# Kernel optimization log

Measured on AMD Instinct MI355X. Metric: run time of the kernel, lower is better.

## Reference

```python
import jax, jax.numpy as jnp
import numpy as np

NUM_EMBEDDINGS = 8192
EMBEDDING_DIM = 256
COMMITMENT_COST = 0.25
TAU = 0.9
B, C, H, W = 4, NUM_EMBEDDINGS, 32, 32


def setup_inputs() -> dict:
    key = jax.random.key(0)
    k1, k2, k3 = jax.random.split(key, 3)
    x = jax.random.normal(k1, (B, C, H, W), dtype=jnp.float32)
    # nn.Embedding weight initialized uniform(-0.5, 0.5)
    emb_weight = jax.random.uniform(k2, (NUM_EMBEDDINGS, EMBEDDING_DIM),
                                    dtype=jnp.float32, minval=-0.5, maxval=0.5)
    # standard Gumbel(0,1) noise, sampled once for reproducibility
    u = jax.random.uniform(k3, (B, C, H, W), dtype=jnp.float32,
                           minval=1e-10, maxval=1.0)
    gumbel_noise = -jnp.log(-jnp.log(u))
    return {"x": x, "emb_weight": emb_weight, "gumbel_noise": gumbel_noise}


def reference(x, emb_weight, gumbel_noise):
    n = x.shape[1]  # num_embeddings (channel dim)
    # --- gumbel_softmax(tau=0.9, hard=True, dim=1) ---
    y_soft = jax.nn.softmax((x + gumbel_noise) / TAU, axis=1)  # [B,N,H,W]
    idx = jnp.argmax(y_soft, axis=1)                           # [B,H,W]
    y_hard = jax.nn.one_hot(idx, n, axis=1, dtype=y_soft.dtype)
    # straight-through estimator
    one_hot = y_soft + jax.lax.stop_gradient(y_hard - y_soft)  # [B,N,H,W]
    # --- codebook lookup as one-hot matmul ---
    quantized = jnp.einsum('bnhw,nd->bdhw', one_hot, emb_weight)
    # --- KL(uniform || q) with F.kl_div semantics, reduction='batchmean' ---
    # logits rearranged to b (h w) n and log_softmax over n == log_softmax over axis=1 of x
    log_qy = jax.nn.log_softmax(x, axis=1)                     # [B,N,H,W]
    t = 1.0 / n
    # pointwise kl = target * (log(target) - log_qy); batchmean divides by B
    kl_div = jnp.sum(t * (jnp.log(jnp.asarray(t, x.dtype)) - log_qy)) / x.shape[0]
    return quantized, COMMITMENT_COST * kl_div, one_hot
```

## Files before the change

### kernel.cpp

```cpp
#include <hip/hip_runtime.h>
#include <math.h>

#define BSZ 4
#define CCH 8192
#define HW  1024
#define DEMB 256
#define NPOS (BSZ*HW)
#define QSIZE (BSZ*DEMB*HW)
#define KLOFF QSIZE
#define OHOFF (QSIZE+1)
#define OHSZ  ((size_t)BSZ*CCH*HW)

typedef float vf4 __attribute__((ext_vector_type(4)));

template<int CPB>
__global__ __launch_bounds__(256) void vq_phase1(const float* __restrict__ x,
                                                 const float* __restrict__ g,
                                                 float* __restrict__ out,
                                                 float* __restrict__ ws) {
    constexpr int NCH = CCH / CPB;
    constexpr int P   = NPOS * NCH;
    constexpr int UN  = 16;
    int bid = blockIdx.x;
    int q = bid % NCH;
    int b = bid / NCH;
    int t = threadIdx.x;
    int c0 = q * CPB;
    size_t base = ((size_t)(b * CCH + c0)) * HW + 4 * t;

    float best[4]; int bidx[4]; float s[4], sx[4];
#pragma unroll
    for (int j = 0; j < 4; j++) { best[j] = -INFINITY; bidx[j] = 0; s[j] = 0.f; sx[j] = 0.f; }

    const vf4 z4 = (vf4)(0.f);
    for (int cg = 0; cg < CPB / UN; cg++) {
        size_t a0 = base + (size_t)cg * UN * HW;
        vf4 xv[UN], gv[UN];
#pragma unroll
        for (int u = 0; u < UN; u++)
            xv[u] = __builtin_nontemporal_load((const vf4*)(x + a0 + (size_t)u * HW));
#pragma unroll
        for (int u = 0; u < UN; u++)
            gv[u] = __builtin_nontemporal_load((const vf4*)(g + a0 + (size_t)u * HW));
#pragma unroll
        for (int u = 0; u < UN; u++)
            __builtin_nontemporal_store(z4, (vf4*)(out + QSIZE + a0 + (size_t)u * HW));
#pragma unroll
        for (int u = 0; u < UN; u++) {
            int cc = c0 + cg * UN + u;
#pragma unroll
            for (int j = 0; j < 4; j++) {
                float xa = xv[u][j];
                float z = xa + gv[u][j];
                if (z > best[j]) { best[j] = z; bidx[j] = cc; }
                s[j]  += __expf(xa);
                sx[j] += xa;
            }
        }
    }

    if (b == BSZ - 1 && q == NCH - 1 && t == 255)
        out[QSIZE + OHSZ] = 0.f;

    int o = q * NPOS + b * HW + 4 * t;
    float* wbest = ws;
    int*   widx  = (int*)(ws + (size_t)P);
    float* wsum  = ws + 2 * (size_t)P;
    float* wsx   = ws + 3 * (size_t)P;
    *(float4*)(wbest + o) = make_float4(best[0], best[1], best[2], best[3]);
    *(int4*)  (widx  + o) = make_int4(bidx[0], bidx[1], bidx[2], bidx[3]);
    *(float4*)(wsum  + o) = make_float4(s[0], s[1], s[2], s[3]);
    *(float4*)(wsx   + o) = make_float4(sx[0], sx[1], sx[2], sx[3]);
}

template<int CPB>
__global__ __launch_bounds__(256) void vq_phase2(const float* __restrict__ emb,
                                                 float* __restrict__ out,
                                                 float* __restrict__ ws) {
    constexpr int NCH = CCH / CPB;
    constexpr int P   = NPOS * NCH;
    constexpr int QPT = NCH / 16;
    constexpr int TP  = 272;
    const float* wbest = ws;
    const int*   widx  = (const int*)(ws + (size_t)P);
    const float* wsum  = ws + 2 * (size_t)P;
    const float* wsx   = ws + 3 * (size_t)P;

    int tid = threadIdx.x;
    int pl = tid & 15;
    int qg = tid >> 4;
    int pos0 = blockIdx.x * 16;
    int pos = pos0 + pl;

    float fb = -INFINITY; int fi = 0;
    float fs = 0.f, fsx = 0.f;
    for (int i = 0; i < QPT; i++) {
        int q = qg * QPT + i;
        int o = q * NPOS + pos;
        float v = wbest[o]; int ci = widx[o];
        if (v > fb || (v == fb && ci < fi)) { fb = v; fi = ci; }
        fs  += wsum[o];
        fsx += wsx[o];
    }

    __shared__ float l_b [16][17];
    __shared__ int   l_i [16][17];
    __shared__ float l_s [16][17];
    __shared__ float l_sx[16][17];
    __shared__ float tsum[16];
    __shared__ int   smi[16];
    __shared__ float tile[16 * TP];
    l_b [qg][pl] = fb;
    l_i [qg][pl] = fi;
    l_s [qg][pl] = fs;
    l_sx[qg][pl] = fsx;
    __syncthreads();

    if (tid < 16) {
        int p = tid;
        float mb = l_b[0][p]; int mi = l_i[0][p];
        float ms = l_s[0][p], msx = l_sx[0][p];
        for (int qq = 1; qq < 16; qq++) {
            float v = l_b[qq][p]; int ci = l_i[qq][p];
            if (v > mb || (v == mb && ci < mi)) { mb = v; mi = ci; }
            ms  += l_s[qq][p];
            msx += l_sx[qq][p];
        }
        int mypos = pos0 + p;
        smi[p] = mi;
        int bb = mypos >> 10;
        int hw = mypos & (HW - 1);
        out[OHOFF + ((size_t)(bb * CCH + mi)) * HW + hw] = 1.0f;

        const float logt = -9.0109131783f;
        tsum[p] = logt + __logf(ms) - msx * (1.0f / (float)CCH);
    }
    __syncthreads();
    if (tid == 0) {
        float tt = 0.f;
        for (int p = 0; p < 16; p++) tt += tsum[p];
        atomicAdd(out + KLOFF, (0.25f / (float)BSZ) * tt);
    }

    int rr = tid >> 6;
    int c4 = (tid & 63) * 4;
#pragma unroll
    for (int rep = 0; rep < 4; rep++) {
        int r = rep * 4 + rr;
        float4 v = *(const float4*)(emb + (size_t)smi[r] * DEMB + c4);
        *(float4*)(tile + r * TP + c4) = v;
    }
    __syncthreads();

    int b = pos0 >> 10;
    int hw0 = pos0 & (HW - 1);
    int d = tid;
    size_t obase = (((size_t)(b * DEMB + d)) << 10) + hw0;
#pragma unroll
    for (int k = 0; k < 4; k++) {
        float4 v;
        v.x = tile[(4 * k + 0) * TP + d];
        v.y = tile[(4 * k + 1) * TP + d];
        v.z = tile[(4 * k + 2) * TP + d];
        v.w = tile[(4 * k + 3) * TP + d];
        *(float4*)(out + obase + 4 * k) = v;
    }
}

template<int CPB>
static void launch_all(const float* x, const float* emb, const float* g,
                       float* out, float* ws, hipStream_t stream) {
    constexpr int NCH = CCH / CPB;
    vq_phase1<CPB><<<dim3(BSZ * NCH), dim3(256), 0, stream>>>(x, g, out, ws);
    vq_phase2<CPB><<<dim3(NPOS / 16), dim3(256), 0, stream>>>(emb, out, ws);
}

extern "C" void kernel_launch(void* const* d_in, const int* in_sizes, int n_in,
                              void* d_out, int out_size, void* d_ws, size_t ws_size,
                              hipStream_t stream) {
    (void)in_sizes; (void)n_in; (void)out_size;
    const float* x   = (const float*)d_in[0];
    const float* emb = (const float*)d_in[1];
    const float* g   = (const float*)d_in[2];
    float* out = (float*)d_out;
    float* ws  = (float*)d_ws;

    if (ws_size >= (size_t)16 * ((size_t)NPOS * (CCH / 32))) {
        launch_all<32>(x, emb, g, out, ws, stream);
    } else {
        launch_all<64>(x, emb, g, out, ws, stream);
    }
}
```

Before: 325.1 us.

## Split phase1 blocks over spatial halves with float2 loads and cooperative zero stores

Measured after the change: 352.2 us. 8.3% more time.

```diff
diff --git a/kernel.cpp b/kernel.cpp
--- a/kernel.cpp
+++ b/kernel.cpp
@@ -12,6 +12,7 @@
 #define OHSZ  ((size_t)BSZ*CCH*HW)
 
 typedef float vf4 __attribute__((ext_vector_type(4)));
+typedef float vf2 __attribute__((ext_vector_type(2)));
 
 template<int CPB>
 __global__ __launch_bounds__(256) void vq_phase1(const float* __restrict__ x,
@@ -21,35 +22,46 @@
     constexpr int NCH = CCH / CPB;
     constexpr int P   = NPOS * NCH;
     constexpr int UN  = 16;
+    constexpr int HHW = HW / 2;
     int bid = blockIdx.x;
-    int q = bid % NCH;
-    int b = bid / NCH;
+    int h  = bid & 1;
+    int qb = bid >> 1;
+    int q = qb % NCH;
+    int b = qb / NCH;
     int t = threadIdx.x;
     int c0 = q * CPB;
-    size_t base = ((size_t)(b * CCH + c0)) * HW + 4 * t;
-
-    float best[4]; int bidx[4]; float s[4], sx[4];
-#pragma unroll
-    for (int j = 0; j < 4; j++) { best[j] = -INFINITY; bidx[j] = 0; s[j] = 0.f; sx[j] = 0.f; }
+    int hw0 = h * HHW;
+    size_t base = ((size_t)(b * CCH + c0)) * HW + hw0 + 2 * t;
+
+    float best[2]; int bidx[2]; float s[2], sx[2];
+#pragma unroll
+    for (int j = 0; j < 2; j++) { best[j] = -INFINITY; bidx[j] = 0; s[j] = 0.f; sx[j] = 0.f; }
 
     const vf4 z4 = (vf4)(0.f);
     for (int cg = 0; cg < CPB / UN; cg++) {
         size_t a0 = base + (size_t)cg * UN * HW;
-        vf4 xv[UN], gv[UN];
+        vf2 xv[UN], gv[UN];
 #pragma unroll
         for (int u = 0; u < UN; u++)
-            xv[u] = __builtin_nontemporal_load((const vf4*)(x + a0 + (size_t)u * HW));
+            xv[u] = *(const vf2*)(x + a0 + (size_t)u * HW);
 #pragma unroll
         for (int u = 0; u < UN; u++)
-            gv[u] = __builtin_nontemporal_load((const vf4*)(g + a0 + (size_t)u * HW));
-#pragma unroll
-        for (int u = 0; u < UN; u++)
-            __builtin_nontemporal_store(z4, (vf4*)(out + QSIZE + a0 + (size_t)u * HW));
+            gv[u] = *(const vf2*)(g + a0 + (size_t)u * HW);
+
+        size_t zb = ((size_t)(b * CCH + c0 + cg * UN)) * HW + hw0;
+#pragma unroll
+        for (int k = 0; k < 8; k++) {
+            int flat = k * 256 + t;
+            int cl   = flat >> 7;
+            int off4 = (flat & 127) * 4;
+            __builtin_nontemporal_store(z4, (vf4*)(out + QSIZE + zb + (size_t)cl * HW + off4));
+        }
+
 #pragma unroll
         for (int u = 0; u < UN; u++) {
             int cc = c0 + cg * UN + u;
 #pragma unroll
-            for (int j = 0; j < 4; j++) {
+            for (int j = 0; j < 2; j++) {
                 float xa = xv[u][j];
                 float z = xa + gv[u][j];
                 if (z > best[j]) { best[j] = z; bidx[j] = cc; }
@@ -59,18 +71,18 @@
         }
     }
 
-    if (b == BSZ - 1 && q == NCH - 1 && t == 255)
+    if (b == BSZ - 1 && q == NCH - 1 && h == 1 && t == 255)
         out[QSIZE + OHSZ] = 0.f;
 
-    int o = q * NPOS + b * HW + 4 * t;
+    int o = q * NPOS + b * HW + hw0 + 2 * t;
     float* wbest = ws;
     int*   widx  = (int*)(ws + (size_t)P);
     float* wsum  = ws + 2 * (size_t)P;
     float* wsx   = ws + 3 * (size_t)P;
-    *(float4*)(wbest + o) = make_float4(best[0], best[1], best[2], best[3]);
-    *(int4*)  (widx  + o) = make_int4(bidx[0], bidx[1], bidx[2], bidx[3]);
-    *(float4*)(wsum  + o) = make_float4(s[0], s[1], s[2], s[3]);
-    *(float4*)(wsx   + o) = make_float4(sx[0], sx[1], sx[2], sx[3]);
+    *(float2*)(wbest + o) = make_float2(best[0], best[1]);
+    *(int2*)  (widx  + o) = make_int2(bidx[0], bidx[1]);
+    *(float2*)(wsum  + o) = make_float2(s[0], s[1]);
+    *(float2*)(wsx   + o) = make_float2(sx[0], sx[1]);
 }
 
 template<int CPB>
@@ -171,7 +183,7 @@
 static void launch_all(const float* x, const float* emb, const float* g,
                        float* out, float* ws, hipStream_t stream) {
     constexpr int NCH = CCH / CPB;
-    vq_phase1<CPB><<<dim3(BSZ * NCH), dim3(256), 0, stream>>>(x, g, out, ws);
+    vq_phase1<CPB><<<dim3(BSZ * NCH * 2), dim3(256), 0, stream>>>(x, g, out, ws);
     vq_phase2<CPB><<<dim3(NPOS / 16), dim3(256), 0, stream>>>(emb, out, ws);
 }
 
```

## Replace per-chunk partial workspace with global atomic max/add reduction

Applied to the files above, without the earlier changes.

Result: slower. 383.5 us (+18.0%).

```diff
diff --git a/kernel.cpp b/kernel.cpp
--- a/kernel.cpp
+++ b/kernel.cpp
@@ -12,6 +12,13 @@
 #define OHSZ  ((size_t)BSZ*CCH*HW)
 
 typedef float vf4 __attribute__((ext_vector_type(4)));
+typedef unsigned long long u64;
+
+
+__global__ __launch_bounds__(256) void vq_init(float* __restrict__ ws) {
+    int i = blockIdx.x * 256 + threadIdx.x;
+    ((vf4*)ws)[i] = (vf4)(0.f);
+}
 
 template<int CPB>
 __global__ __launch_bounds__(256) void vq_phase1(const float* __restrict__ x,
@@ -19,7 +26,6 @@
                                                  float* __restrict__ out,
                                                  float* __restrict__ ws) {
     constexpr int NCH = CCH / CPB;
-    constexpr int P   = NPOS * NCH;
     constexpr int UN  = 16;
     int bid = blockIdx.x;
     int q = bid % NCH;
@@ -62,78 +68,47 @@
     if (b == BSZ - 1 && q == NCH - 1 && t == 255)
         out[QSIZE + OHSZ] = 0.f;
 
-    int o = q * NPOS + b * HW + 4 * t;
-    float* wbest = ws;
-    int*   widx  = (int*)(ws + (size_t)P);
-    float* wsum  = ws + 2 * (size_t)P;
-    float* wsx   = ws + 3 * (size_t)P;
-    *(float4*)(wbest + o) = make_float4(best[0], best[1], best[2], best[3]);
-    *(int4*)  (widx  + o) = make_int4(bidx[0], bidx[1], bidx[2], bidx[3]);
-    *(float4*)(wsum  + o) = make_float4(s[0], s[1], s[2], s[3]);
-    *(float4*)(wsx   + o) = make_float4(sx[0], sx[1], sx[2], sx[3]);
+    u64*   pk  = (u64*)ws;
+    float* ps  = ws + 2 * (size_t)NPOS;
+    float* psx = ws + 3 * (size_t)NPOS;
+    int p0 = b * HW + 4 * t;
+#pragma unroll
+    for (int j = 0; j < 4; j++) {
+        unsigned ub  = __float_as_uint(best[j]);
+        unsigned key = (ub & 0x80000000u) ? ~ub : (ub | 0x80000000u);
+        u64 v = ((u64)key << 32) | (unsigned)(CCH - 1 - bidx[j]);
+        atomicMax(&pk[p0 + j], v);
+        atomicAdd(&ps[p0 + j], s[j]);
+        atomicAdd(&psx[p0 + j], sx[j]);
+    }
 }
 
-template<int CPB>
 __global__ __launch_bounds__(256) void vq_phase2(const float* __restrict__ emb,
                                                  float* __restrict__ out,
-                                                 float* __restrict__ ws) {
-    constexpr int NCH = CCH / CPB;
-    constexpr int P   = NPOS * NCH;
-    constexpr int QPT = NCH / 16;
-    constexpr int TP  = 272;
-    const float* wbest = ws;
-    const int*   widx  = (const int*)(ws + (size_t)P);
-    const float* wsum  = ws + 2 * (size_t)P;
-    const float* wsx   = ws + 3 * (size_t)P;
+                                                 const float* __restrict__ ws) {
+    constexpr int TP = 272;
+    const u64*   pk  = (const u64*)ws;
+    const float* ps  = ws + 2 * (size_t)NPOS;
+    const float* psx = ws + 3 * (size_t)NPOS;
 
-    int tid = threadIdx.x;
-    int pl = tid & 15;
-    int qg = tid >> 4;
+    __shared__ int   smi[16];
+    __shared__ float tsum[16];
+    __shared__ float tile[16 * TP];
+
+    int tid  = threadIdx.x;
     int pos0 = blockIdx.x * 16;
-    int pos = pos0 + pl;
-
-    float fb = -INFINITY; int fi = 0;
-    float fs = 0.f, fsx = 0.f;
-    for (int i = 0; i < QPT; i++) {
-        int q = qg * QPT + i;
-        int o = q * NPOS + pos;
-        float v = wbest[o]; int ci = widx[o];
-        if (v > fb || (v == fb && ci < fi)) { fb = v; fi = ci; }
-        fs  += wsum[o];
-        fsx += wsx[o];
-    }
-
-    __shared__ float l_b [16][17];
-    __shared__ int   l_i [16][17];
-    __shared__ float l_s [16][17];
-    __shared__ float l_sx[16][17];
-    __shared__ float tsum[16];
-    __shared__ int   smi[16];
-    __shared__ float tile[16 * TP];
-    l_b [qg][pl] = fb;
-    l_i [qg][pl] = fi;
-    l_s [qg][pl] = fs;
-    l_sx[qg][pl] = fsx;
-    __syncthreads();
 
     if (tid < 16) {
-        int p = tid;
-        float mb = l_b[0][p]; int mi = l_i[0][p];
-        float ms = l_s[0][p], msx = l_sx[0][p];
-        for (int qq = 1; qq < 16; qq++) {
-            float v = l_b[qq][p]; int ci = l_i[qq][p];
-            if (v > mb || (v == mb && ci < mi)) { mb = v; mi = ci; }
-            ms  += l_s[qq][p];
-            msx += l_sx[qq][p];
-        }
-        int mypos = pos0 + p;
-        smi[p] = mi;
-        int bb = mypos >> 10;
-        int hw = mypos & (HW - 1);
+        int pos = pos0 + tid;
+        u64 v = pk[pos];
+        int mi = (CCH - 1) - (int)(unsigned)(v & 0xFFFFFFFFu);
+        smi[tid] = mi;
+        int bb = pos >> 10;
+        int hw = pos & (HW - 1);
         out[OHOFF + ((size_t)(bb * CCH + mi)) * HW + hw] = 1.0f;
 
         const float logt = -9.0109131783f;
-        tsum[p] = logt + __logf(ms) - msx * (1.0f / (float)CCH);
+        tsum[tid] = logt + __logf(ps[pos]) - psx[pos] * (1.0f / (float)CCH);
     }
     __syncthreads();
     if (tid == 0) {
@@ -167,27 +142,18 @@
     }
 }
 
-template<int CPB>
-static void launch_all(const float* x, const float* emb, const float* g,
-                       float* out, float* ws, hipStream_t stream) {
-    constexpr int NCH = CCH / CPB;
-    vq_phase1<CPB><<<dim3(BSZ * NCH), dim3(256), 0, stream>>>(x, g, out, ws);
-    vq_phase2<CPB><<<dim3(NPOS / 16), dim3(256), 0, stream>>>(emb, out, ws);
-}
-
 extern "C" void kernel_launch(void* const* d_in, const int* in_sizes, int n_in,
                               void* d_out, int out_size, void* d_ws, size_t ws_size,
                               hipStream_t stream) {
-    (void)in_sizes; (void)n_in; (void)out_size;
+    (void)in_sizes; (void)n_in; (void)out_size; (void)ws_size;
     const float* x   = (const float*)d_in[0];
     const float* emb = (const float*)d_in[1];
     const float* g   = (const float*)d_in[2];
     float* out = (float*)d_out;
     float* ws  = (float*)d_ws;
 
-    if (ws_size >= (size_t)16 * ((size_t)NPOS * (CCH / 32))) {
-        launch_all<32>(x, emb, g, out, ws, stream);
-    } else {
-        launch_all<64>(x, emb, g, out, ws, stream);
-    }
+    vq_init<<<dim3(16), dim3(256), 0, stream>>>(ws);
+
+    vq_phase1<32><<<dim3(BSZ * (CCH / 32)), dim3(256), 0, stream>>>(x, g, out, ws);
+    vq_phase2<<<dim3(NPOS / 16), dim3(256), 0, stream>>>(emb, out, ws);
 }
```
